# Kernel optimization log

Measured on AMD Instinct MI355X. Metric: run time of the kernel, lower is better.

## Reference

```python
import jax, jax.numpy as jnp
import numpy as np

FEATURE_LIST = [222, 27, 373, 283, 26, 7]
EMB_HID = 6
TN, UN, TF = 2000, 50000, 16


def setup_inputs() -> dict:
    key = jax.random.key(0)
    ks = jax.random.split(key, 4 + len(FEATURE_LIST))
    T_static = jax.random.normal(ks[0], (TN, TF), dtype=jnp.float32)
    # per-column categorical indices, each in-range for its table
    cols = [jax.random.randint(jax.random.fold_in(ks[1], i), (UN,), 0, sz)
            for i, sz in enumerate(FEATURE_LIST)]
    U_static = jnp.stack(cols, axis=1).astype(jnp.int64)  # [UN, 6]
    team_user_matrix = jax.random.randint(ks[2], (TN, UN), 0, 2, dtype=jnp.int32)
    inp = {"T_static": T_static, "U_static": U_static,
           "team_user_matrix": team_user_matrix}
    # embedding tables, xavier_uniform with gain=sqrt(2)
    for i, sz in enumerate(FEATURE_LIST):
        bound = np.sqrt(2.0) * np.sqrt(6.0 / (sz + EMB_HID))
        inp[f"emb{i}"] = jax.random.uniform(ks[3 + i], (sz, EMB_HID),
                                            minval=-bound, maxval=bound,
                                            dtype=jnp.float32)
    return inp


def reference(T_static, U_static, team_user_matrix,
              emb0, emb1, emb2, emb3, emb4, emb5):
    tables = [emb0, emb1, emb2, emb3, emb4, emb5]
    # gather per-feature embeddings and concat -> [UN, 6*emb_hid]
    U_emb = jnp.concatenate(
        [t[U_static[:, i]] for i, t in enumerate(tables)], axis=-1)
    mask = (team_user_matrix == 1).astype(U_emb.dtype)        # [TN, UN]
    counts = jnp.sum(mask, axis=1, keepdims=True)             # [TN, 1]
    # masked mean over each team's users == (mask @ U_emb) / counts
    T_emb = jnp.matmul(mask, U_emb) / counts                  # [TN, 36]
    return jnp.concatenate([T_static, T_emb], axis=-1)        # [TN, TF+36]
```

## Files before the change

### kernel.cpp

```cpp
#include <hip/hip_runtime.h>
#include <hip/hip_bf16.h>

#define TN 2000
#define UN 50000
#define TF 16
#define NCOL 48
#define UNP 50016
#define KSTEPS 1563
#define KFULL 1562
#define KCHUNKS 48
#define SPC 33
#define MTILES 125

typedef __attribute__((ext_vector_type(8))) short short8;
typedef __attribute__((ext_vector_type(4))) float f32x4;

__device__ inline unsigned short f2bf(float f) {
    unsigned int x = __float_as_uint(f);
    x += 0x7FFFu + ((x >> 16) & 1u);
    return (unsigned short)(x >> 16);
}

__global__ void build_uembT(const int* __restrict__ U,
                            const float* __restrict__ e0, const float* __restrict__ e1,
                            const float* __restrict__ e2, const float* __restrict__ e3,
                            const float* __restrict__ e4, const float* __restrict__ e5,
                            unsigned short* __restrict__ UT) {
    int u = blockIdx.x * 256 + threadIdx.x;
    int c = blockIdx.y;
    if (u >= UNP) return;
    unsigned short val = 0;
    if (u < UN) {
        if (c < 36) {
            int f = c / 6, h = c - f * 6;
            const float* t = (f == 0) ? e0 : (f == 1) ? e1 : (f == 2) ? e2
                           : (f == 3) ? e3 : (f == 4) ? e4 : e5;
            int idx = U[u * 6 + f];
            val = f2bf(t[idx * 6 + h]);
        } else if (c == 36) {
            val = 0x3F80;
        }
    }
    UT[(size_t)c * UNP + u] = val;
}

__device__ inline short8 mask_to_bf16(const int v[8]) {
    union { short8 s; int i[4]; } a;
    #pragma unroll
    for (int j = 0; j < 4; ++j) {
        int lo = (v[2 * j]     == 1) ? 0x3F80     : 0;
        int hi = (v[2 * j + 1] == 1) ? 0x3F800000 : 0;
        a.i[j] = lo | hi;
    }
    return a.s;
}

__global__ __launch_bounds__(256) void masked_gemm(
        const int* __restrict__ mask, const unsigned short* __restrict__ UT,
        float* __restrict__ partial) {
    int wave = threadIdx.x >> 6;
    int lane = threadIdx.x & 63;
    int mtile = blockIdx.x * 4 + wave;
    if (mtile >= MTILES) return;
    int m0 = mtile * 16;
    int r  = lane & 15;
    int g8 = (lane >> 4) * 8;
    int ky = blockIdx.y;

    int ks0 = ky * SPC;
    int ks1 = ks0 + SPC; if (ks1 > KSTEPS) ks1 = KSTEPS;
    int ksf = (ks1 < KFULL) ? ks1 : KFULL;

    f32x4 acc0 = {0.f, 0.f, 0.f, 0.f};
    f32x4 acc1 = {0.f, 0.f, 0.f, 0.f};
    f32x4 acc2 = {0.f, 0.f, 0.f, 0.f};

    const int* arow = mask + (size_t)(m0 + r) * UN + g8;
    const unsigned short* b0 = UT + (size_t)(r)      * UNP + g8;
    const unsigned short* b1 = UT + (size_t)(r + 16) * UNP + g8;
    const unsigned short* b2 = UT + (size_t)(r + 32) * UNP + g8;

    #pragma unroll 3
    for (int ks = ks0; ks < ksf; ++ks) {
        int gk = ks * 32;
        const int4* p = (const int4*)(arow + gk);
        int4 v0 = p[0], v1 = p[1];
        int v[8] = {v0.x, v0.y, v0.z, v0.w, v1.x, v1.y, v1.z, v1.w};
        short8 a  = mask_to_bf16(v);
        short8 f0 = *(const short8*)(b0 + gk);
        short8 f1 = *(const short8*)(b1 + gk);
        short8 f2 = *(const short8*)(b2 + gk);
        acc0 = __builtin_amdgcn_mfma_f32_16x16x32_bf16(a, f0, acc0, 0, 0, 0);
        acc1 = __builtin_amdgcn_mfma_f32_16x16x32_bf16(a, f1, acc1, 0, 0, 0);
        acc2 = __builtin_amdgcn_mfma_f32_16x16x32_bf16(a, f2, acc2, 0, 0, 0);
    }
    if (ks1 > KFULL) {
        int gk = KFULL * 32;
        short8 a = {0,0,0,0,0,0,0,0};
        if (g8 < 16) {
            const int4* p = (const int4*)(arow + gk);
            int4 v0 = p[0], v1 = p[1];
            int v[8] = {v0.x, v0.y, v0.z, v0.w, v1.x, v1.y, v1.z, v1.w};
            a = mask_to_bf16(v);
        }
        short8 f0 = *(const short8*)(b0 + gk);
        short8 f1 = *(const short8*)(b1 + gk);
        short8 f2 = *(const short8*)(b2 + gk);
        acc0 = __builtin_amdgcn_mfma_f32_16x16x32_bf16(a, f0, acc0, 0, 0, 0);
        acc1 = __builtin_amdgcn_mfma_f32_16x16x32_bf16(a, f1, acc1, 0, 0, 0);
        acc2 = __builtin_amdgcn_mfma_f32_16x16x32_bf16(a, f2, acc2, 0, 0, 0);
    }

    int row0 = m0 + (lane >> 4) * 4;
    int col  = lane & 15;
    float* out = partial + ((size_t)ky * TN) * NCOL;
    #pragma unroll
    for (int reg = 0; reg < 4; ++reg) {
        size_t rb = (size_t)(row0 + reg) * NCOL;
        out[rb + col]      = acc0[reg];
        out[rb + col + 16] = acc1[reg];
        out[rb + col + 32] = acc2[reg];
    }
}

__global__ void finalize(const float* __restrict__ T_static,
                         const float* __restrict__ partial,
                         float* __restrict__ out) {
    int t = blockIdx.x;
    int c = threadIdx.x;
    if (c >= TF + 36) return;
    float v;
    if (c < TF) {
        v = T_static[(size_t)t * TF + c];
    } else {
        int n = c - TF;
        float s = 0.f, cnt = 0.f;
        #pragma unroll 4
        for (int ky = 0; ky < KCHUNKS; ++ky) {
            const float* row = partial + ((size_t)ky * TN + t) * NCOL;
            s   += row[n];
            cnt += row[36];
        }
        v = s / cnt;
    }
    out[(size_t)t * (TF + 36) + c] = v;
}

extern "C" void kernel_launch(void* const* d_in, const int* in_sizes, int n_in,
                              void* d_out, int out_size, void* d_ws, size_t ws_size,
                              hipStream_t stream) {
    const float* T_static = (const float*)d_in[0];
    const int*   U_static = (const int*)d_in[1];
    const int*   mask     = (const int*)d_in[2];
    const float* e0 = (const float*)d_in[3];
    const float* e1 = (const float*)d_in[4];
    const float* e2 = (const float*)d_in[5];
    const float* e3 = (const float*)d_in[6];
    const float* e4 = (const float*)d_in[7];
    const float* e5 = (const float*)d_in[8];
    float* out = (float*)d_out;

    unsigned short* UT = (unsigned short*)d_ws;
    size_t ut_bytes = (size_t)NCOL * UNP * sizeof(unsigned short);
    float* partial = (float*)((char*)d_ws + ut_bytes);

    build_uembT<<<dim3((UNP + 255) / 256, NCOL), dim3(256), 0, stream>>>(
        U_static, e0, e1, e2, e3, e4, e5, UT);
    masked_gemm<<<dim3(32, KCHUNKS), dim3(256), 0, stream>>>(mask, UT, partial);
    finalize<<<dim3(TN), dim3(64), 0, stream>>>(T_static, partial, out);
}
```

Before: 587.5 us.

## Software-prefetch mask/UT loads, use nontemporal mask loads, and reorder partial layout

The main GEMM loop now double-buffers its operands: it loads the next K-step's mask and UT fragments before converting and multiplying the current ones. This is meant to hide global-load latency. Mask loads use nontemporal hints so the large streamed matrix does less cache pollution. The partial buffer is reordered to [team][chunk][col], and only the 37 used columns are stored, so finalize reads contiguous memory. The risks are higher register pressure and the loss of the previous unroll.

```diff
diff --git a/kernel.cpp b/kernel.cpp
--- a/kernel.cpp
+++ b/kernel.cpp
@@ -14,6 +14,7 @@
 
 typedef __attribute__((ext_vector_type(8))) short short8;
 typedef __attribute__((ext_vector_type(4))) float f32x4;
+typedef __attribute__((ext_vector_type(4))) int i32x4;
 
 __device__ inline unsigned short f2bf(float f) {
     unsigned int x = __float_as_uint(f);
@@ -44,14 +45,12 @@
     UT[(size_t)c * UNP + u] = val;
 }
 
-__device__ inline short8 mask_to_bf16(const int v[8]) {
+__device__ inline short8 mask_to_bf16(i32x4 v0, i32x4 v1) {
     union { short8 s; int i[4]; } a;
-    #pragma unroll
-    for (int j = 0; j < 4; ++j) {
-        int lo = (v[2 * j]     == 1) ? 0x3F80     : 0;
-        int hi = (v[2 * j + 1] == 1) ? 0x3F800000 : 0;
-        a.i[j] = lo | hi;
-    }
+    a.i[0] = ((v0.x == 1) ? 0x3F80 : 0) | ((v0.y == 1) ? 0x3F800000 : 0);
+    a.i[1] = ((v0.z == 1) ? 0x3F80 : 0) | ((v0.w == 1) ? 0x3F800000 : 0);
+    a.i[2] = ((v1.x == 1) ? 0x3F80 : 0) | ((v1.y == 1) ? 0x3F800000 : 0);
+    a.i[3] = ((v1.z == 1) ? 0x3F80 : 0) | ((v1.w == 1) ? 0x3F800000 : 0);
     return a.s;
 }
 
@@ -80,46 +79,61 @@
     const unsigned short* b1 = UT + (size_t)(r + 16) * UNP + g8;
     const unsigned short* b2 = UT + (size_t)(r + 32) * UNP + g8;
 
-    #pragma unroll 3
-    for (int ks = ks0; ks < ksf; ++ks) {
-        int gk = ks * 32;
-        const int4* p = (const int4*)(arow + gk);
-        int4 v0 = p[0], v1 = p[1];
-        int v[8] = {v0.x, v0.y, v0.z, v0.w, v1.x, v1.y, v1.z, v1.w};
-        short8 a  = mask_to_bf16(v);
-        short8 f0 = *(const short8*)(b0 + gk);
-        short8 f1 = *(const short8*)(b1 + gk);
-        short8 f2 = *(const short8*)(b2 + gk);
-        acc0 = __builtin_amdgcn_mfma_f32_16x16x32_bf16(a, f0, acc0, 0, 0, 0);
-        acc1 = __builtin_amdgcn_mfma_f32_16x16x32_bf16(a, f1, acc1, 0, 0, 0);
-        acc2 = __builtin_amdgcn_mfma_f32_16x16x32_bf16(a, f2, acc2, 0, 0, 0);
+    int gk = ks0 * 32;
+    const i32x4* pa = (const i32x4*)(arow + gk);
+    i32x4 va0 = __builtin_nontemporal_load(pa);
+    i32x4 va1 = __builtin_nontemporal_load(pa + 1);
+    short8 fb0 = *(const short8*)(b0 + gk);
+    short8 fb1 = *(const short8*)(b1 + gk);
+    short8 fb2 = *(const short8*)(b2 + gk);
+
+    for (int ks = ks0; ks < ksf - 1; ++ks) {
+        i32x4 ca0 = va0, ca1 = va1;
+        short8 cb0 = fb0, cb1 = fb1, cb2 = fb2;
+        int gn = (ks + 1) * 32;
+        const i32x4* pn = (const i32x4*)(arow + gn);
+        va0 = __builtin_nontemporal_load(pn);
+        va1 = __builtin_nontemporal_load(pn + 1);
+        fb0 = *(const short8*)(b0 + gn);
+        fb1 = *(const short8*)(b1 + gn);
+        fb2 = *(const short8*)(b2 + gn);
+        short8 a = mask_to_bf16(ca0, ca1);
+        acc0 = __builtin_amdgcn_mfma_f32_16x16x32_bf16(a, cb0, acc0, 0, 0, 0);
+        acc1 = __builtin_amdgcn_mfma_f32_16x16x32_bf16(a, cb1, acc1, 0, 0, 0);
+        acc2 = __builtin_amdgcn_mfma_f32_16x16x32_bf16(a, cb2, acc2, 0, 0, 0);
+    }
+    {
+        short8 a = mask_to_bf16(va0, va1);
+        acc0 = __builtin_amdgcn_mfma_f32_16x16x32_bf16(a, fb0, acc0, 0, 0, 0);
+        acc1 = __builtin_amdgcn_mfma_f32_16x16x32_bf16(a, fb1, acc1, 0, 0, 0);
+        acc2 = __builtin_amdgcn_mfma_f32_16x16x32_bf16(a, fb2, acc2, 0, 0, 0);
     }
     if (ks1 > KFULL) {
-        int gk = KFULL * 32;
+        int tk = KFULL * 32;
         short8 a = {0,0,0,0,0,0,0,0};
         if (g8 < 16) {
-            const int4* p = (const int4*)(arow + gk);
-            int4 v0 = p[0], v1 = p[1];
-            int v[8] = {v0.x, v0.y, v0.z, v0.w, v1.x, v1.y, v1.z, v1.w};
-            a = mask_to_bf16(v);
+            const i32x4* p = (const i32x4*)(arow + tk);
+            i32x4 v0 = __builtin_nontemporal_load(p);
+            i32x4 v1 = __builtin_nontemporal_load(p + 1);
+            a = mask_to_bf16(v0, v1);
         }
-        short8 f0 = *(const short8*)(b0 + gk);
-        short8 f1 = *(const short8*)(b1 + gk);
-        short8 f2 = *(const short8*)(b2 + gk);
-        acc0 = __builtin_amdgcn_mfma_f32_16x16x32_bf16(a, f0, acc0, 0, 0, 0);
-        acc1 = __builtin_amdgcn_mfma_f32_16x16x32_bf16(a, f1, acc1, 0, 0, 0);
-        acc2 = __builtin_amdgcn_mfma_f32_16x16x32_bf16(a, f2, acc2, 0, 0, 0);
+        short8 t0 = *(const short8*)(b0 + tk);
+        short8 t1 = *(const short8*)(b1 + tk);
+        short8 t2 = *(const short8*)(b2 + tk);
+        acc0 = __builtin_amdgcn_mfma_f32_16x16x32_bf16(a, t0, acc0, 0, 0, 0);
+        acc1 = __builtin_amdgcn_mfma_f32_16x16x32_bf16(a, t1, acc1, 0, 0, 0);
+        acc2 = __builtin_amdgcn_mfma_f32_16x16x32_bf16(a, t2, acc2, 0, 0, 0);
     }
 
     int row0 = m0 + (lane >> 4) * 4;
     int col  = lane & 15;
-    float* out = partial + ((size_t)ky * TN) * NCOL;
     #pragma unroll
     for (int reg = 0; reg < 4; ++reg) {
-        size_t rb = (size_t)(row0 + reg) * NCOL;
-        out[rb + col]      = acc0[reg];
-        out[rb + col + 16] = acc1[reg];
-        out[rb + col + 32] = acc2[reg];
+        size_t rb = ((size_t)(row0 + reg) * KCHUNKS + ky) * NCOL;
+        partial[rb + col]      = acc0[reg];
+        partial[rb + col + 16] = acc1[reg];
+        if (col < 5)
+            partial[rb + col + 32] = acc2[reg];
     }
 }
 
@@ -134,12 +148,12 @@
         v = T_static[(size_t)t * TF + c];
     } else {
         int n = c - TF;
+        const float* base = partial + (size_t)t * KCHUNKS * NCOL;
         float s = 0.f, cnt = 0.f;
-        #pragma unroll 4
+        #pragma unroll 6
         for (int ky = 0; ky < KCHUNKS; ++ky) {
-            const float* row = partial + ((size_t)ky * TN + t) * NCOL;
-            s   += row[n];
-            cnt += row[36];
+            s   += base[ky * NCOL + n];
+            cnt += base[ky * NCOL + 36];
         }
         v = s / cnt;
     }
```

Measured after the change: 621.4 us. 5.8% more time.
